# Kernel optimization log

Measured on AMD Instinct MI355X. Metric: run time of the kernel, lower is better.

The kernel has to match this reference:

```python
import jax, jax.numpy as jnp
import numpy as np

B, T, C = 4, 2048, 768
H, D = 12, 64          # num heads, head size
MLP = 3072
EPS = 1e-6
SCALE = C ** (-0.5)    # NOTE: source scales by n_embd**-0.5, not head_size**-0.5


def setup_inputs() -> dict:
    key = jax.random.key(0)
    ks = jax.random.split(key, 12)
    s = 0.02
    return {
        "x":     jax.random.normal(ks[0], (B, T, C), jnp.float32),
        "Wq":    jax.random.normal(ks[1], (H, C, D), jnp.float32) * s,
        "Wk":    jax.random.normal(ks[2], (H, C, D), jnp.float32) * s,
        "Wv":    jax.random.normal(ks[3], (H, C, D), jnp.float32) * s,
        "Wo":    jax.random.normal(ks[4], (H * D, C), jnp.float32) * s,
        "bo":    jnp.zeros((C,), jnp.float32),
        "ln1_g": jnp.ones((C,), jnp.float32),
        "ln1_b": jnp.zeros((C,), jnp.float32),
        "ln2_g": jnp.ones((C,), jnp.float32),
        "ln2_b": jnp.zeros((C,), jnp.float32),
        "W1":    jax.random.normal(ks[5], (C, MLP), jnp.float32) * s,
        "b1":    jnp.zeros((MLP,), jnp.float32),
        "W2":    jax.random.normal(ks[6], (MLP, C), jnp.float32) * s,
        "b2":    jnp.zeros((C,), jnp.float32),
    }


def _ln(x, g, b):
    mu = jnp.mean(x, axis=-1, keepdims=True)
    var = jnp.var(x, axis=-1, keepdims=True)
    return (x - mu) * jax.lax.rsqrt(var + EPS) * g + b


def reference(x, Wq, Wk, Wv, Wo, bo, ln1_g, ln1_b, ln2_g, ln2_b, W1, b1, W2, b2):
    xn = _ln(x, ln1_g, ln1_b)
    # batched per-head projections: [B,T,C] x [H,C,D] -> [B,H,T,D]
    q = jnp.einsum("btc,hcd->bhtd", xn, Wq)
    k = jnp.einsum("btc,hcd->bhtd", xn, Wk)
    v = jnp.einsum("btc,hcd->bhtd", xn, Wv)
    wei = jnp.einsum("bhtd,bhsd->bhts", q, k) * SCALE  # [B,H,T,T]
    wei = jax.nn.softmax(wei, axis=-1)
    attn = jnp.einsum("bhts,bhsd->bhtd", wei, v)
    # concat heads along feature dim (head order preserved)
    attn = attn.transpose(0, 2, 1, 3).reshape(B, T, H * D)
    sa = attn @ Wo + bo
    x2 = sa + x                      # residual 1 (dropout = identity in eval)
    y = _ln(x2, ln2_g, ln2_b)
    y = jax.nn.gelu(y @ W1 + b1, approximate=False) @ W2 + b2
    return x2 + y                    # residual 2
```

## Files before the change

kernel.cpp:

```cpp
#include <hip/hip_runtime.h>
#include <hip/hip_bf16.h>
#include <cstdint>
#include <cmath>

#define B_ 4
#define T_ 2048
#define C_ 768
#define H_ 12
#define D_ 64
#define MLP_ 3072
#define BT_ (B_*T_)

typedef __hip_bfloat16 hbf;
typedef __bf16 bf16_t;
typedef bf16_t bf16x8 __attribute__((ext_vector_type(8)));
typedef bf16_t bf16x4 __attribute__((ext_vector_type(4)));
typedef float f32x4 __attribute__((ext_vector_type(4)));

static __device__ __forceinline__ void load_lds16(const void* g, void* l) {
    __builtin_amdgcn_global_load_lds(
        (const __attribute__((address_space(1))) unsigned int*)g,
        (__attribute__((address_space(3))) unsigned int*)l, 16, 0, 0);
}

__global__ __launch_bounds__(256) void pack_ln(
    const float* __restrict__ x, const float* __restrict__ ln1g,
    const float* __restrict__ ln1b, hbf* __restrict__ xn,
    const float* __restrict__ Wq, const float* __restrict__ Wk,
    const float* __restrict__ Wv, const float* __restrict__ Wo,
    const float* __restrict__ W1, const float* __restrict__ W2,
    hbf* __restrict__ WqkT, hbf* __restrict__ WoT,
    hbf* __restrict__ W1T, hbf* __restrict__ W2T)
{
    __shared__ float smem[64 * 65];
    const int blk = blockIdx.x;
    const int t = threadIdx.x;
    if (blk < 8192) {
        const bool act = t < 192;
        float v[4] = {0, 0, 0, 0};
        if (act) {
            const float4 xv = *(const float4*)(x + (size_t)blk * C_ + t * 4);
            v[0] = xv.x; v[1] = xv.y; v[2] = xv.z; v[3] = xv.w;
        }
        float s = 0.0f, s2 = 0.0f;
#pragma unroll
        for (int k = 0; k < 4; ++k) { s += v[k]; s2 += v[k] * v[k]; }
#pragma unroll
        for (int m = 1; m < 64; m <<= 1) {
            s  += __shfl_xor(s,  m, 64);
            s2 += __shfl_xor(s2, m, 64);
        }
        if (act && (t & 63) == 0) { smem[t >> 6] = s; smem[3 + (t >> 6)] = s2; }
        __syncthreads();
        if (act) {
            float S  = smem[0] + smem[1] + smem[2];
            float S2 = smem[3] + smem[4] + smem[5];
            float mu  = S * (1.0f / C_);
            float var = S2 * (1.0f / C_) - mu * mu;
            float inv = rsqrtf(var + 1e-6f);
            const float4 gv = *(const float4*)(ln1g + t * 4);
            const float4 bv = *(const float4*)(ln1b + t * 4);
            bf16x4 o4;
            o4[0] = (bf16_t)((v[0] - mu) * inv * gv.x + bv.x);
            o4[1] = (bf16_t)((v[1] - mu) * inv * gv.y + bv.y);
            o4[2] = (bf16_t)((v[2] - mu) * inv * gv.z + bv.z);
            o4[3] = (bf16_t)((v[3] - mu) * inv * gv.w + bv.w);
            *(bf16x4*)((bf16_t*)xn + (size_t)blk * C_ + t * 4) = o4;
        }
        return;
    }
    const int pb = blk - 8192;
    const float* src; hbf* dst; int R, S, r0, s0;
    if (pb < 432) {
        const int z = pb / 12, y = pb - z * 12;
        const int mtx = z / 12, head = z - mtx * 12;
        src = (mtx == 0 ? Wq : mtx == 1 ? Wk : Wv) + (size_t)head * 49152;
        dst = WqkT + (size_t)z * 49152;
        R = 768; S = 64; r0 = y * 64; s0 = 0;
    } else if (pb < 576) {
        const int l = pb - 432;
        src = Wo; dst = WoT; R = 768; S = 768;
        r0 = (l / 12) * 64; s0 = (l % 12) * 64;
    } else if (pb < 1152) {
        const int l = pb - 576;
        src = W1; dst = W1T; R = 768; S = 3072;
        r0 = (l / 48) * 64; s0 = (l % 48) * 64;
    } else {
        const int l = pb - 1152;
        src = W2; dst = W2T; R = 3072; S = 768;
        r0 = (l / 12) * 64; s0 = (l % 12) * 64;
    }
    const int c = t & 63, q = t >> 6;
#pragma unroll
    for (int j = 0; j < 16; ++j) {
        int r = q + j * 4;
        smem[r * 65 + c] = src[(size_t)(r0 + r) * S + s0 + c];
    }
    __syncthreads();
#pragma unroll
    for (int j = 0; j < 16; ++j) {
        int s = q + j * 4;
        dst[(size_t)(s0 + s) * R + r0 + c] = __float2bfloat16(smem[c * 65 + s]);
    }
}

template<typename TI>
__global__ __launch_bounds__(192) void ln_kernel(
    const TI* __restrict__ x, const float* __restrict__ g,
    const float* __restrict__ bb, hbf* __restrict__ out)
{
    __shared__ float red[6];
    const int row = blockIdx.x;
    const int t = threadIdx.x;
    float v[4];
    if constexpr (__is_same(TI, float)) {
        const float4 xv = *(const float4*)(x + (size_t)row * C_ + t * 4);
        v[0] = xv.x; v[1] = xv.y; v[2] = xv.z; v[3] = xv.w;
    } else {
        bf16x4 xv = *(const bf16x4*)((const bf16_t*)x + (size_t)row * C_ + t * 4);
#pragma unroll
        for (int k = 0; k < 4; ++k) v[k] = (float)xv[k];
    }
    float s = 0.0f, s2 = 0.0f;
#pragma unroll
    for (int k = 0; k < 4; ++k) { s += v[k]; s2 += v[k] * v[k]; }
#pragma unroll
    for (int m = 1; m < 64; m <<= 1) {
        s  += __shfl_xor(s,  m, 64);
        s2 += __shfl_xor(s2, m, 64);
    }
    if ((t & 63) == 0) { red[t >> 6] = s; red[3 + (t >> 6)] = s2; }
    __syncthreads();
    float S  = red[0] + red[1] + red[2];
    float S2 = red[3] + red[4] + red[5];
    float mu  = S * (1.0f / C_);
    float var = S2 * (1.0f / C_) - mu * mu;
    float inv = rsqrtf(var + 1e-6f);
    const float4 gv = *(const float4*)(g  + t * 4);
    const float4 bv = *(const float4*)(bb + t * 4);
    bf16x4 o4;
    o4[0] = (bf16_t)((v[0] - mu) * inv * gv.x + bv.x);
    o4[1] = (bf16_t)((v[1] - mu) * inv * gv.y + bv.y);
    o4[2] = (bf16_t)((v[2] - mu) * inv * gv.z + bv.z);
    o4[3] = (bf16_t)((v[3] - mu) * inv * gv.w + bv.w);
    *(bf16x4*)((bf16_t*)out + (size_t)row * C_ + t * 4) = o4;
}

template<int EPI, int TN>
__global__ __launch_bounds__(256, 4) void gemm_kernel(
    const hbf* __restrict__ A, const hbf* __restrict__ Bt,
    float* __restrict__ outF, hbf* __restrict__ outH,
    const float* __restrict__ bias, const float* __restrict__ residF,
    const hbf* __restrict__ residH,
    int M, int N, int K,
    hbf* __restrict__ qb, hbf* __restrict__ kb, hbf* __restrict__ vt,
    float scale, int gx)
{
    constexpr int AM = (TN == 128) ? 4 : 2;
    constexpr int NB_B = (TN == 128) ? 4 : 2;
    __shared__ hbf sA[128 * 64];
    __shared__ hbf sB[TN * 64];
    const int tid = threadIdx.x;
    const int lane = tid & 63;
    const int wid = tid >> 6;
    const int lr = lane & 15, hg = lane >> 4;
    const int bid = blockIdx.x, nwg = gridDim.x;
    const int wg = (bid & 7) * (nwg >> 3) + (bid >> 3);
    const int bx = wg % gx, by = wg / gx;
    const int row0 = by * 128;
    const int col0 = bx * TN;
    const int wrow = (TN == 128) ? (wid >> 1) * 64 : wid * 32;
    const int wcol = (TN == 128) ? (wid & 1) * 64 : 0;

    f32x4 acc[AM][4] = {};

    int offG[4];
    const int Kb = K * 2;
#pragma unroll
    for (int i = 0; i < 4; ++i) {
        int c = tid + i * 256;
        offG[i] = (c >> 3) * Kb + (((c & 7) ^ ((c >> 3) & 7)) << 4);
    }
    const char* gA = (const char*)(A + (size_t)row0 * K);
    const char* gB = (const char*)(Bt + (size_t)col0 * K);

    auto stage = [&](int kt) {
        const int kb2 = kt * 128;
#pragma unroll
        for (int i = 0; i < 4; ++i)
            load_lds16(gA + (size_t)(offG[i] + kb2), (char*)sA + i * 4096 + wid * 1024);
#pragma unroll
        for (int i = 0; i < NB_B; ++i)
            load_lds16(gB + (size_t)(offG[i] + kb2), (char*)sB + i * 4096 + wid * 1024);
    };

    const int NK = K >> 6;
    stage(0);
    for (int kt = 0; kt < NK; ++kt) {
        __syncthreads();
#pragma unroll
        for (int kf = 0; kf < 2; ++kf) {
            const int sl = ((kf * 4 + hg) ^ (lr & 7)) << 4;
            bf16x8 af[AM], bfr[4];
#pragma unroll
            for (int m = 0; m < AM; ++m)
                af[m] = *(const bf16x8*)((const char*)sA + (wrow + m * 16 + lr) * 128 + sl);
#pragma unroll
            for (int n = 0; n < 4; ++n)
                bfr[n] = *(const bf16x8*)((const char*)sB + (wcol + n * 16 + lr) * 128 + sl);
#pragma unroll
            for (int m = 0; m < AM; ++m)
#pragma unroll
                for (int n = 0; n < 4; ++n)
                    acc[m][n] = __builtin_amdgcn_mfma_f32_16x16x32_bf16(af[m], bfr[n], acc[m][n], 0, 0, 0);
        }
        __syncthreads();
        if (kt + 1 < NK) stage(kt + 1);
    }

#pragma unroll
    for (int m = 0; m < AM; ++m) {
#pragma unroll
        for (int n = 0; n < 4; ++n) {
            const int colc = col0 + wcol + n * 16 + lr;
            const int rowb = row0 + wrow + m * 16 + hg * 4;
            if constexpr (EPI == 3) {
                if (colc >= 2 * C_) {
                    bf16x4 w;
#pragma unroll
                    for (int j = 0; j < 4; ++j) w[j] = (bf16_t)acc[m][n][j];
                    *(bf16x4*)(vt + (size_t)(colc - 2 * C_) * BT_ + rowb) = w;
                    continue;
                }
            }
#pragma unroll
            for (int j = 0; j < 4; ++j) {
                int row = rowb + j;
                int col = colc;
                float v = acc[m][n][j];
                if constexpr (EPI == 0) {
                    outH[(size_t)row * N + col] = __float2bfloat16(v);
                } else if constexpr (EPI == 2) {
                    float tt = v + bias[col];
                    float t3 = tt * tt * tt;
                    float z = fminf(fmaf(t3, 0.1029423372f, 2.3021141876f * tt), 126.0f);
                    float e = __builtin_amdgcn_exp2f(z);
                    float ge = tt * e * __builtin_amdgcn_rcpf(e + 1.0f);
                    outH[(size_t)row * N + col] = __float2bfloat16(ge);
                } else if constexpr (EPI == 3) {
                    int typ = col / C_;
                    int rr = col - typ * C_;
                    int h = rr >> 6, d = rr & 63;
                    int b = row >> 11, t = row & (T_ - 1);
                    size_t bh = (size_t)b * H_ + h;
                    if (typ == 0) qb[(bh * T_ + t) * D_ + d] = __float2bfloat16(v * scale);
                    else          kb[(bh * T_ + t) * D_ + d] = __float2bfloat16(v);
                } else if constexpr (EPI == 4) {
                    outH[(size_t)row * N + col] =
                        __float2bfloat16(v + bias[col] + residF[(size_t)row * N + col]);
                } else {
                    outF[(size_t)row * N + col] =
                        v + bias[col] + __bfloat162float(residH[(size_t)row * N + col]);
                }
            }
        }
    }
}

__global__ __launch_bounds__(256, 3) void attn_kernel(
    const hbf* __restrict__ qg, const hbf* __restrict__ kg,
    const hbf* __restrict__ vg, hbf* __restrict__ outA)
{
    __shared__ hbf sK0[64 * 64], sK1[64 * 64];
    __shared__ hbf sV0[64 * 64], sV1[64 * 64];
    __shared__ hbf sP[4 * 32 * 64];
    const int tid = threadIdx.x, lane = tid & 63, wid = tid >> 6;
    const int lr = lane & 15, hg = lane >> 4;
    const int wg = (blockIdx.x & 7) * 96 + (blockIdx.x >> 3);
    const int bh = wg >> 4;
    const int b = bh / H_, h = bh - b * H_;
    const int wr0 = (wg & 15) * 128 + wid * 32;
    const hbf* qbh = qg + (size_t)bh * T_ * D_;
    const hbf* kbh = kg + (size_t)bh * T_ * D_;
    const hbf* vbh = vg + (size_t)h * 64 * BT_ + (size_t)b * T_;

    bf16x8 a_q[2][2];
#pragma unroll
    for (int m = 0; m < 2; ++m)
#pragma unroll
        for (int kf = 0; kf < 2; ++kf)
            a_q[m][kf] = *(const bf16x8*)(qbh + (size_t)(wr0 + m * 16 + lr) * D_ + kf * 32 + hg * 8);

    bf16x8 vone;
#pragma unroll
    for (int i = 0; i < 8; ++i) vone[i] = (bf16_t)1.0f;

    f32x4 o[2][4] = {};
    f32x4 lden[2] = {};
    float mreg[2] = {-3e38f, -3e38f};

    int offK[2], offV[2];
#pragma unroll
    for (int i = 0; i < 2; ++i) {
        int c = tid + i * 256;
        int sw = ((c & 7) ^ ((c >> 3) & 7)) << 4;
        offK[i] = (c >> 3) * 128 + sw;
        offV[i] = (c >> 3) * (BT_ * 2) + sw;
    }
    hbf* sPw = sP + wid * (32 * 64);
    const int sl0 = ((0 * 4 + hg) ^ (lr & 7)) << 4;
    const int sl1 = ((1 * 4 + hg) ^ (lr & 7)) << 4;
    const int bcast = hg * 20;

    auto stage = [&](int itn, hbf* sKd, hbf* sVd) {
        const char* kp = (const char*)kbh + (size_t)itn * 8192;
        const char* vp = (const char*)vbh + (size_t)itn * 128;
#pragma unroll
        for (int i = 0; i < 2; ++i) {
            load_lds16(kp + offK[i], (char*)sKd + i * 4096 + wid * 1024);
            load_lds16(vp + offV[i], (char*)sVd + i * 4096 + wid * 1024);
        }
    };

#define SOFTMAX_M(m, tmv)                                                      \
    {                                                                          \
        if (__any((tmv) - mreg[m] > 11.5415603f)) {                            \
            float nm = fmaxf(mreg[m], (tmv));                                  \
            float fac = __builtin_amdgcn_exp2f(mreg[m] - nm);                  \
            mreg[m] = nm;                                                      \
            float fb[4];                                                       \
            _Pragma("unroll")                                                  \
            for (int j = 0; j < 4; ++j) fb[j] = __shfl(fac, bcast + j, 64);    \
            _Pragma("unroll")                                                  \
            for (int j = 0; j < 4; ++j) {                                      \
                lden[m][j] *= fb[j];                                           \
                _Pragma("unroll")                                              \
                for (int nd = 0; nd < 4; ++nd) o[m][nd][j] *= fb[j];           \
            }                                                                  \
        }                                                                      \
        const int r = (m) * 16 + lr;                                           \
        _Pragma("unroll")                                                      \
        for (int n = 0; n < 4; ++n) {                                          \
            float p0 = __builtin_amdgcn_exp2f(st[n][m][0] - mreg[m]);          \
            float p1 = __builtin_amdgcn_exp2f(st[n][m][1] - mreg[m]);          \
            float p2 = __builtin_amdgcn_exp2f(st[n][m][2] - mreg[m]);          \
            float p3 = __builtin_amdgcn_exp2f(st[n][m][3] - mreg[m]);          \
            bf16x4 w;                                                          \
            w[0] = (bf16_t)p0; w[1] = (bf16_t)p1;                              \
            w[2] = (bf16_t)p2; w[3] = (bf16_t)p3;                              \
            *(bf16x4*)((char*)sPw + r * 128 +                                  \
                       (((n * 2 + (hg >> 1)) ^ (r & 7)) << 4) +                \
                       ((hg & 1) * 8)) = w;                                    \
        }                                                                      \
    }

#define PV_M(m)                                                                \
    __builtin_amdgcn_s_setprio(1);                                             \
    _Pragma("unroll")                                                          \
    for (int kf = 0; kf < 2; ++kf) {                                           \
        const int sl = kf ? sl1 : sl0;                                         \
        bf16x8 ap = *(const bf16x8*)((const char*)sPw + ((m) * 16 + lr) * 128 + sl); \
        lden[m] = __builtin_amdgcn_mfma_f32_16x16x32_bf16(ap, vone, lden[m], 0, 0, 0); \
        _Pragma("unroll")                                                      \
        for (int nd = 0; nd < 4; ++nd)                                         \
            o[m][nd] = __builtin_amdgcn_mfma_f32_16x16x32_bf16(ap, bvr[kf][nd], o[m][nd], 0, 0, 0); \
    }                                                                          \
    __builtin_amdgcn_s_setprio(0);

    auto tile = [&](const hbf* sKc, const hbf* sVc) {
        f32x4 st[4][2] = {};
        __builtin_amdgcn_s_setprio(1);
#pragma unroll
        for (int kf = 0; kf < 2; ++kf) {
            const int sl = kf ? sl1 : sl0;
#pragma unroll
            for (int n = 0; n < 4; ++n) {
                bf16x8 ak = *(const bf16x8*)((const char*)sKc + (n * 16 + lr) * 128 + sl);
                st[n][0] = __builtin_amdgcn_mfma_f32_16x16x32_bf16(ak, a_q[0][kf], st[n][0], 0, 0, 0);
                st[n][1] = __builtin_amdgcn_mfma_f32_16x16x32_bf16(ak, a_q[1][kf], st[n][1], 0, 0, 0);
            }
        }
        __builtin_amdgcn_s_setprio(0);

        bf16x8 bvr[2][4];
#pragma unroll
        for (int kf = 0; kf < 2; ++kf) {
            const int sl = kf ? sl1 : sl0;
#pragma unroll
            for (int nd = 0; nd < 4; ++nd)
                bvr[kf][nd] = *(const bf16x8*)((const char*)sVc + (nd * 16 + lr) * 128 + sl);
        }

        float tm[2];
#pragma unroll
        for (int m = 0; m < 2; ++m) {
            f32x4 mx = st[0][m];
            mx[0] = fmaxf(mx[0], st[1][m][0]); mx[1] = fmaxf(mx[1], st[1][m][1]);
            mx[2] = fmaxf(mx[2], st[1][m][2]); mx[3] = fmaxf(mx[3], st[1][m][3]);
            f32x4 my = st[2][m];
            my[0] = fmaxf(my[0], st[3][m][0]); my[1] = fmaxf(my[1], st[3][m][1]);
            my[2] = fmaxf(my[2], st[3][m][2]); my[3] = fmaxf(my[3], st[3][m][3]);
            float t01 = fmaxf(fmaxf(mx[0], my[0]), fmaxf(mx[1], my[1]));
            float t23 = fmaxf(fmaxf(mx[2], my[2]), fmaxf(mx[3], my[3]));
            tm[m] = fmaxf(t01, t23);
        }
        {
            float a0 = tm[0], b0 = tm[0], a1 = tm[1], b1 = tm[1];
            asm volatile("v_permlane32_swap_b32 %0, %1" : "+v"(a0), "+v"(b0));
            asm volatile("v_permlane32_swap_b32 %0, %1" : "+v"(a1), "+v"(b1));
            a0 = fmaxf(a0, b0);
            a1 = fmaxf(a1, b1);
            float s0 = __shfl_xor(a0, 16, 64);
            float s1 = __shfl_xor(a1, 16, 64);
            tm[0] = fmaxf(a0, s0);
            tm[1] = fmaxf(a1, s1);
        }

        SOFTMAX_M(0, tm[0]);
        PV_M(0);
        SOFTMAX_M(1, tm[1]);
        PV_M(1);
    };

    const int NT = T_ / 64;
    stage(0, sK0, sV0);
    __syncthreads();
    for (int it = 0; it < NT; it += 2) {
        stage(it + 1, sK1, sV1);
        tile(sK0, sV0);
        __syncthreads();
        if (it + 2 < NT) stage(it + 2, sK0, sV0);
        tile(sK1, sV1);
        __syncthreads();
    }

#pragma unroll
    for (int m = 0; m < 2; ++m) {
        f32x4 rinv;
#pragma unroll
        for (int j = 0; j < 4; ++j) rinv[j] = __builtin_amdgcn_rcpf(lden[m][j]);
#pragma unroll
        for (int nd = 0; nd < 4; ++nd)
#pragma unroll
            for (int j = 0; j < 4; ++j) {
                int row = wr0 + m * 16 + hg * 4 + j;
                int col = nd * 16 + lr;
                outA[((size_t)(b * T_ + row)) * C_ + h * D_ + col] =
                    __float2bfloat16(o[m][nd][j] * rinv[j]);
            }
    }
#undef SOFTMAX_M
#undef PV_M
}

extern "C" void kernel_launch(void* const* d_in, const int* in_sizes, int n_in,
                              void* d_out, int out_size, void* d_ws, size_t ws_size,
                              hipStream_t stream)
{
    const float* x    = (const float*)d_in[0];
    const float* Wq   = (const float*)d_in[1];
    const float* Wk   = (const float*)d_in[2];
    const float* Wv   = (const float*)d_in[3];
    const float* Wo   = (const float*)d_in[4];
    const float* bo   = (const float*)d_in[5];
    const float* ln1g = (const float*)d_in[6];
    const float* ln1b = (const float*)d_in[7];
    const float* ln2g = (const float*)d_in[8];
    const float* ln2b = (const float*)d_in[9];
    const float* W1   = (const float*)d_in[10];
    const float* b1   = (const float*)d_in[11];
    const float* W2   = (const float*)d_in[12];
    const float* b2   = (const float*)d_in[13];
    float* out = (float*)d_out;
    char* ws = (char*)d_ws;

    hbf*  xn    = (hbf*)(ws + 0);
    hbf*  WqkT  = (hbf*)(ws + 12582912);
    hbf*  qb    = (hbf*)(ws + 16121856);
    hbf*  kb    = (hbf*)(ws + 28704768);
    hbf*  vT    = (hbf*)(ws + 41287680);
    hbf*  h1    = (hbf*)(ws + 0);
    hbf*  attnB = (hbf*)(ws + 53870592);
    hbf*  yln   = (hbf*)(ws + 53870592);
    hbf*  x2b   = (hbf*)(ws + 66453504);
    hbf*  WoT   = (hbf*)(ws + 91619328);
    hbf*  W1T   = (hbf*)(ws + 92798976);
    hbf*  W2T   = (hbf*)(ws + 97517568);

    const float SCALE2 = 0.036084391824351615f * 1.4426950408889634f;

    pack_ln<<<9920, 256, 0, stream>>>(x, ln1g, ln1b, xn,
        Wq, Wk, Wv, Wo, W1, W2, WqkT, WoT, W1T, W2T);
    gemm_kernel<3,128><<<1152, 256, 0, stream>>>(xn, WqkT, nullptr, nullptr, nullptr, nullptr,
        nullptr, 8192, 2304, 768, qb, kb, vT, SCALE2, 18);
    attn_kernel<<<768, 256, 0, stream>>>(qb, kb, vT, attnB);
    gemm_kernel<4,64><<<768, 256, 0, stream>>>(attnB, WoT, nullptr, x2b, bo, x,
        nullptr, 8192, 768, 768, nullptr, nullptr, nullptr, 1.0f, 12);
    ln_kernel<hbf><<<8192, 192, 0, stream>>>(x2b, ln2g, ln2b, yln);
    gemm_kernel<2,128><<<1536, 256, 0, stream>>>(yln, W1T, nullptr, h1, b1, nullptr,
        nullptr, 8192, 3072, 768, nullptr, nullptr, nullptr, 1.0f, 24);
    gemm_kernel<5,64><<<768, 256, 0, stream>>>(h1, W2T, out, nullptr, b2, nullptr,
        x2b, 8192, 768, 3072, nullptr, nullptr, nullptr, 1.0f, 12);
}
```

Measured before the change: 257.7 us.

## Use dedicated 256x128-tile, 512-thread GEMM for the MLP up-projection

Adds a new gemm_big kernel with 256x128 output tiles, 8 waves each computing a 64x64 sub-tile, and the GELU+bias epilogue. It replaces the generic 128-tile GEMM for the W1 projection. The larger tile raises arithmetic intensity per LDS load and halves the block count. It keeps single-buffered LDS with two barriers per k-step, so load latency is not overlapped, and the launch bounds ask for high occupancy with 48KB of LDS per block.

```diff
diff --git a/kernel.cpp b/kernel.cpp
--- a/kernel.cpp
+++ b/kernel.cpp
@@ -240,13 +240,6 @@
                 float v = acc[m][n][j];
                 if constexpr (EPI == 0) {
                     outH[(size_t)row * N + col] = __float2bfloat16(v);
-                } else if constexpr (EPI == 2) {
-                    float tt = v + bias[col];
-                    float t3 = tt * tt * tt;
-                    float z = fminf(fmaf(t3, 0.1029423372f, 2.3021141876f * tt), 126.0f);
-                    float e = __builtin_amdgcn_exp2f(z);
-                    float ge = tt * e * __builtin_amdgcn_rcpf(e + 1.0f);
-                    outH[(size_t)row * N + col] = __float2bfloat16(ge);
                 } else if constexpr (EPI == 3) {
                     int typ = col / C_;
                     int rr = col - typ * C_;
@@ -262,6 +255,95 @@
                     outF[(size_t)row * N + col] =
                         v + bias[col] + __bfloat162float(residH[(size_t)row * N + col]);
                 }
+            }
+        }
+    }
+}
+
+__global__ __launch_bounds__(512, 4) void gemm_big(
+    const hbf* __restrict__ A, const hbf* __restrict__ Bt,
+    hbf* __restrict__ outH, const float* __restrict__ bias,
+    int M, int N, int K, int gx)
+{
+    __shared__ hbf sA[256 * 64];
+    __shared__ hbf sB[128 * 64];
+    const int tid = threadIdx.x;
+    const int lane = tid & 63;
+    const int wid = tid >> 6;
+    const int lr = lane & 15, hg = lane >> 4;
+    const int bid = blockIdx.x, nwg = gridDim.x;
+    const int wg = (bid & 7) * (nwg >> 3) + (bid >> 3);
+    const int bx = wg % gx, by = wg / gx;
+    const int row0 = by * 256;
+    const int col0 = bx * 128;
+    const int wrow = (wid >> 1) * 64;
+    const int wcol = (wid & 1) * 64;
+
+    f32x4 acc[4][4] = {};
+
+    int offGA[4], offGB[2];
+    const int Kb = K * 2;
+#pragma unroll
+    for (int i = 0; i < 4; ++i) {
+        int c = tid + i * 512;
+        offGA[i] = (c >> 3) * Kb + (((c & 7) ^ ((c >> 3) & 7)) << 4);
+    }
+#pragma unroll
+    for (int i = 0; i < 2; ++i) {
+        int c = tid + i * 512;
+        offGB[i] = (c >> 3) * Kb + (((c & 7) ^ ((c >> 3) & 7)) << 4);
+    }
+    const char* gA = (const char*)(A + (size_t)row0 * K);
+    const char* gB = (const char*)(Bt + (size_t)col0 * K);
+
+    auto stage = [&](int kt) {
+        const int kb2 = kt * 128;
+#pragma unroll
+        for (int i = 0; i < 4; ++i)
+            load_lds16(gA + (size_t)(offGA[i] + kb2), (char*)sA + i * 8192 + wid * 1024);
+#pragma unroll
+        for (int i = 0; i < 2; ++i)
+            load_lds16(gB + (size_t)(offGB[i] + kb2), (char*)sB + i * 8192 + wid * 1024);
+    };
+
+    const int NK = K >> 6;
+    stage(0);
+    for (int kt = 0; kt < NK; ++kt) {
+        __syncthreads();
+#pragma unroll
+        for (int kf = 0; kf < 2; ++kf) {
+            const int sl = ((kf * 4 + hg) ^ (lr & 7)) << 4;
+            bf16x8 af[4], bfr[4];
+#pragma unroll
+            for (int m = 0; m < 4; ++m)
+                af[m] = *(const bf16x8*)((const char*)sA + (wrow + m * 16 + lr) * 128 + sl);
+#pragma unroll
+            for (int n = 0; n < 4; ++n)
+                bfr[n] = *(const bf16x8*)((const char*)sB + (wcol + n * 16 + lr) * 128 + sl);
+#pragma unroll
+            for (int m = 0; m < 4; ++m)
+#pragma unroll
+                for (int n = 0; n < 4; ++n)
+                    acc[m][n] = __builtin_amdgcn_mfma_f32_16x16x32_bf16(af[m], bfr[n], acc[m][n], 0, 0, 0);
+        }
+        __syncthreads();
+        if (kt + 1 < NK) stage(kt + 1);
+    }
+
+#pragma unroll
+    for (int m = 0; m < 4; ++m) {
+#pragma unroll
+        for (int n = 0; n < 4; ++n) {
+            const int col = col0 + wcol + n * 16 + lr;
+            const int rowb = row0 + wrow + m * 16 + hg * 4;
+#pragma unroll
+            for (int j = 0; j < 4; ++j) {
+                float tt = acc[m][n][j] + bias[col];
+                float t3 = tt * tt * tt;
+                float z = fminf(fmaf(t3, 0.1029423372f, 2.3021141876f * tt), 126.0f);
+                float e = __builtin_amdgcn_exp2f(z);
+                float ge = tt * e * __builtin_amdgcn_rcpf(e + 1.0f);
+                outH[(size_t)(rowb + j) * N + col] = __float2bfloat16(ge);
             }
         }
     }
@@ -497,8 +579,7 @@
     gemm_kernel<4,64><<<768, 256, 0, stream>>>(attnB, WoT, nullptr, x2b, bo, x,
         nullptr, 8192, 768, 768, nullptr, nullptr, nullptr, 1.0f, 12);
     ln_kernel<hbf><<<8192, 192, 0, stream>>>(x2b, ln2g, ln2b, yln);
-    gemm_kernel<2,128><<<1536, 256, 0, stream>>>(yln, W1T, nullptr, h1, b1, nullptr,
-        nullptr, 8192, 3072, 768, nullptr, nullptr, nullptr, 1.0f, 24);
+    gemm_big<<<768, 512, 0, stream>>>(yln, W1T, h1, b1, 8192, 3072, 768, 24);
     gemm_kernel<5,64><<<768, 256, 0, stream>>>(h1, W2T, out, nullptr, b2, nullptr,
         x2b, 8192, 768, 3072, nullptr, nullptr, nullptr, 1.0f, 12);
 }
```

Result: no change. 259.1 us (+0.5%).
